# Performance work log

Hardware: AMD Instinct MI355X
Metric: run time of the kernel (lower is better)

Reference implementation:

```python
import jax, jax.numpy as jnp
import numpy as np

N_NODES = 50000
N_EDGES = 800000
N_FEAT = 128
HIDDEN = 128
N_CLASSES = 10
N_GRAPHS = 100


def setup_inputs() -> dict:
    key = jax.random.key(0)
    ks = jax.random.split(key, 16)
    x = jax.random.normal(ks[0], (N_NODES, N_FEAT), dtype=jnp.float32)
    edge_index = jax.random.randint(ks[1], (2, N_EDGES), 0, N_NODES, dtype=jnp.int64)
    batch = jnp.sort(jax.random.randint(ks[2], (N_NODES,), 0, N_GRAPHS, dtype=jnp.int64))

    def glorot(k, fi, fo):
        s = jnp.sqrt(6.0 / (fi + fo)).astype(jnp.float32)
        return jax.random.uniform(k, (fi, fo), jnp.float32, -s, s)

    return {
        "x": x,
        "edge_index": edge_index,
        "batch": batch,
        "W1": glorot(ks[3], N_FEAT, HIDDEN),
        "b1": jnp.zeros((HIDDEN,), jnp.float32),
        "W2": glorot(ks[4], HIDDEN, HIDDEN),
        "b2": jnp.zeros((HIDDEN,), jnp.float32),
        "W3": glorot(ks[5], HIDDEN, HIDDEN // 2),
        "b3": jnp.zeros((HIDDEN // 2,), jnp.float32),
        "Wf1": glorot(ks[6], HIDDEN // 2, 32),
        "bf1": jnp.zeros((32,), jnp.float32),
        "Wf2": glorot(ks[7], 32, N_CLASSES),
        "bf2": jnp.zeros((N_CLASSES,), jnp.float32),
    }


def _gcn_conv(x, row, col, norm, W, b, n_nodes):
    # GCNConv: x' = D^{-1/2}(A+I)D^{-1/2} (x W) + b
    h = x @ W                                            # [N, out]
    msg = h[row] * norm[:, None]                         # gather + scale per edge
    out = jax.ops.segment_sum(msg, col, num_segments=n_nodes)  # scatter-add to targets
    return out + b


def reference(x, edge_index, batch, W1, b1, W2, b2, W3, b3, Wf1, bf1, Wf2, bf2):
    n = x.shape[0]
    # add self-loops (PyG GCNConv default)
    loop = jnp.arange(n, dtype=edge_index.dtype)
    row = jnp.concatenate([edge_index[0], loop])
    col = jnp.concatenate([edge_index[1], loop])
    # symmetric normalization from in-degree at targets (edge_weight = 1)
    deg = jax.ops.segment_sum(jnp.ones_like(col, x.dtype), col, num_segments=n)
    dinv = jnp.where(deg > 0, jax.lax.rsqrt(deg), 0.0)
    norm = dinv[row] * dinv[col]                         # [E + N]

    h = jax.nn.relu(_gcn_conv(x, row, col, norm, W1, b1, n))
    h = jax.nn.relu(_gcn_conv(h, row, col, norm, W2, b2, n))
    h = jax.nn.relu(_gcn_conv(h, row, col, norm, W3, b3, n))

    # global_mean_pool over graphs
    sums = jax.ops.segment_sum(h, batch, num_segments=N_GRAPHS)
    cnts = jax.ops.segment_sum(jnp.ones((n,), h.dtype), batch, num_segments=N_GRAPHS)
    pooled = sums / jnp.maximum(cnts, 1.0)[:, None]      # [G, hidden//2]

    h = jax.nn.relu(pooled @ Wf1 + bf1)
    logits = h @ Wf2 + bf2                               # [G, num_classes]
    return logits
```

## Files before the change

kernel.cpp:

```cpp
#include <hip/hip_runtime.h>
#include <hip/hip_fp16.h>


#define NGRAPH 100
#define CAP 64

typedef _Float16 f16x8 __attribute__((ext_vector_type(8)));
typedef float f32x4 __attribute__((ext_vector_type(4)));


__global__ __launch_bounds__(256) void prep_all(const float* __restrict__ W1,
                                                const float* __restrict__ W2,
                                                const float* __restrict__ W3,
                                                __half* __restrict__ Wt1,
                                                __half* __restrict__ Wt2,
                                                __half* __restrict__ Wt3,
                                                int* __restrict__ cnt,
                                                float* __restrict__ pooled, int n) {
    const int idx = blockIdx.x * 256 + threadIdx.x;
    if (idx < 16384) {
        int nn = idx >> 7, k = idx & 127;
        Wt1[idx] = __float2half(W1[k * 128 + nn]);
    } else if (idx < 32768) {
        int j = idx - 16384;
        int nn = j >> 7, k = j & 127;
        Wt2[j] = __float2half(W2[k * 128 + nn]);
    } else if (idx < 40960) {
        int j = idx - 32768;
        int nn = j >> 7, k = j & 127;
        Wt3[j] = __float2half(W3[k * 64 + nn]);
    }
    if (idx < n) cnt[idx] = 0;
    if (idx < NGRAPH * 64) pooled[idx] = 0.0f;
}


__global__ void fill_bucket(const int* __restrict__ row, const int* __restrict__ col,
                            int* __restrict__ cnt, int* __restrict__ bucket,
                            int E, int colsPerGroup) {
    const int g  = blockIdx.x & 7;
    const int gb = blockIdx.x >> 3;
    const int nb = gridDim.x >> 3;
    const int lo = g * colsPerGroup, hi = lo + colsPerGroup;
    for (int e = gb * 256 + threadIdx.x; e < E; e += nb * 256) {
        int c = col[e];
        if (c >= lo && c < hi) {
            int pos = atomicAdd(&cnt[c], 1);
            bucket[c * CAP + pos] = row[e];
        }
    }
}


template <int OUT, bool F16IN>
__global__ __launch_bounds__(256) void gemm_mfma(const void* __restrict__ Xv,
                                                 const __half* __restrict__ Wt,
                                                 const float* __restrict__ bias_in,
                                                 const int* __restrict__ cnt,
                                                 __half* __restrict__ Yh, int n) {
    __shared__ _Float16 Xs[64 * 128];
    __shared__ _Float16 Ws[OUT * 128];
    __shared__ float bs[128];

    const float*  Xf = (const float*)Xv;
    const __half* Xh = (const __half*)Xv;

    const int t = threadIdx.x;
    if (t < 128) bs[t] = (bias_in != nullptr) ? bias_in[t] : 0.0f;
    __syncthreads();

    const int row0 = blockIdx.x * 64;
    const bool do_relu = (bias_in != nullptr);

    for (int c = t; c < 64 * 16; c += 256) {
        const int r = c >> 4, q = c & 15;
        const int gr = row0 + r;
        float vals[8];
        #pragma unroll
        for (int i = 0; i < 8; ++i) vals[i] = 0.0f;
        if (gr < n) {
            if (F16IN) {
                f16x8 hv = *(const f16x8*)&Xh[(size_t)gr * 128 + q * 8];
                #pragma unroll
                for (int i = 0; i < 8; ++i) vals[i] = (float)hv[i];
            } else {
                float4 va = *(const float4*)&Xf[(size_t)gr * 128 + q * 8];
                float4 vb = *(const float4*)&Xf[(size_t)gr * 128 + q * 8 + 4];
                vals[0] = va.x; vals[1] = va.y; vals[2] = va.z; vals[3] = va.w;
                vals[4] = vb.x; vals[5] = vb.y; vals[6] = vb.z; vals[7] = vb.w;
            }
        }
        if (do_relu) {
            const int k = q * 8;
            #pragma unroll
            for (int i = 0; i < 8; ++i) vals[i] = fmaxf(vals[i] + bs[k + i], 0.f);
        }
        f16x8 hv;
        #pragma unroll
        for (int i = 0; i < 8; ++i) hv[i] = (_Float16)vals[i];
        *(f16x8*)&Xs[(size_t)((r << 4) + (q ^ (r & 15))) * 8] = hv;
    }
    for (int c = t; c < OUT * 16; c += 256) {
        const int nn = c >> 4, q = c & 15;
        f16x8 w = *(const f16x8*)&Wt[nn * 128 + q * 8];
        *(f16x8*)&Ws[(size_t)((nn << 4) + (q ^ (nn & 15))) * 8] = w;
    }
    __syncthreads();

    constexpr int NT = OUT / 16;
    const int lane = t & 63, wave = t >> 6;
    const int m = lane & 15, quad = lane >> 4;

    f32x4 acc[NT];
    #pragma unroll
    for (int i = 0; i < NT; ++i) acc[i] = (f32x4){0.f, 0.f, 0.f, 0.f};

    #pragma unroll
    for (int s = 0; s < 4; ++s) {
        const int qa = s * 4 + quad;
        f16x8 a = *(const f16x8*)&Xs[(size_t)(((wave * 16 + m) << 4) + (qa ^ m)) * 8];
        #pragma unroll
        for (int tt = 0; tt < NT; ++tt) {
            f16x8 b = *(const f16x8*)&Ws[(size_t)(((tt * 16 + m) << 4) + (qa ^ m)) * 8];
            acc[tt] = __builtin_amdgcn_mfma_f32_16x16x32_f16(a, b, acc[tt], 0, 0, 0);
        }
    }

    #pragma unroll
    for (int i = 0; i < 4; ++i) {
        const int gr = row0 + wave * 16 + quad * 4 + i;
        if (gr < n) {
            const float dw = 1.0f / sqrtf((float)(cnt[gr] + 1));
            #pragma unroll
            for (int tt = 0; tt < NT; ++tt)
                Yh[(size_t)gr * OUT + tt * 16 + m] = __float2half(acc[tt][i] * dw);
        }
    }
}


template <int F>
__global__ void gather_kernel(const __half* __restrict__ hs, const int* __restrict__ cnt,
                              const int* __restrict__ bucket,
                              __half* __restrict__ outh, int n) {
    const int lane = threadIdx.x & 63;
    const int c = (blockIdx.x * blockDim.x + threadIdx.x) >> 6;
    if (c >= n) return;
    const int beg = c * CAP;
    const int end = beg + cnt[c];
    const float w = 1.0f / sqrtf((float)(cnt[c] + 1));
    const float2* hq = (const float2*)hs;

    auto cvt = [](float2 raw) {
        __half2 ha = *(__half2*)&raw.x;
        __half2 hb = *(__half2*)&raw.y;
        float2 fa = __half22float2(ha);
        float2 fb = __half22float2(hb);
        return make_float4(fa.x, fa.y, fb.x, fb.y);
    };
    auto pack = [](float4 v) {
        float2 o;
        *(__half2*)&o.x = __float22half2_rn(make_float2(v.x, v.y));
        *(__half2*)&o.y = __float22half2_rn(make_float2(v.z, v.w));
        return o;
    };

    if (F == 128) {
        const int half = lane >> 5;
        const int l    = lane & 31;
        float4 acc = make_float4(0.f, 0.f, 0.f, 0.f);
        if (half == 0) acc = cvt(hq[(size_t)c * 32 + l]);
        int j = beg + half;
        for (; j + 6 < end; j += 8) {
            int s0 = bucket[j], s1 = bucket[j + 2], s2 = bucket[j + 4], s3 = bucket[j + 6];
            float4 v0 = cvt(hq[(size_t)s0 * 32 + l]);
            float4 v1 = cvt(hq[(size_t)s1 * 32 + l]);
            float4 v2 = cvt(hq[(size_t)s2 * 32 + l]);
            float4 v3 = cvt(hq[(size_t)s3 * 32 + l]);
            acc.x += v0.x + v1.x + v2.x + v3.x;
            acc.y += v0.y + v1.y + v2.y + v3.y;
            acc.z += v0.z + v1.z + v2.z + v3.z;
            acc.w += v0.w + v1.w + v2.w + v3.w;
        }
        for (; j < end; j += 2) {
            float4 v = cvt(hq[(size_t)bucket[j] * 32 + l]);
            acc.x += v.x; acc.y += v.y; acc.z += v.z; acc.w += v.w;
        }
        acc.x += __shfl(acc.x, lane ^ 32);
        acc.y += __shfl(acc.y, lane ^ 32);
        acc.z += __shfl(acc.z, lane ^ 32);
        acc.w += __shfl(acc.w, lane ^ 32);
        if (half == 0) {
            float4 o = make_float4(w * acc.x, w * acc.y, w * acc.z, w * acc.w);
            *(float2*)&outh[(size_t)c * 128 + l * 4] = pack(o);
        }
    }
}


__global__ __launch_bounds__(256) void fused_gpool(const __half* __restrict__ hs,
                                                   const int* __restrict__ cnt,
                                                   const int* __restrict__ bucket,
                                                   const float* __restrict__ b3,
                                                   const int* __restrict__ batch,
                                                   float* __restrict__ pooled, int n) {
    const int lane  = threadIdx.x & 63;
    const int half  = lane >> 5;
    const int li    = lane & 31;
    const int wave  = (blockIdx.x * blockDim.x + threadIdx.x) >> 6;
    const int nwav  = (gridDim.x * blockDim.x) >> 6;
    const int chunk = (n + nwav - 1) / nwav;
    const int beg = wave * chunk;
    const int end = min(beg + chunk, n);
    if (beg >= end) return;
    const unsigned* h2 = (const unsigned*)hs;

    auto cvt2 = [](unsigned raw) { return __half22float2(*(__half2*)&raw); };

    const float bias0 = b3[li * 2], bias1 = b3[li * 2 + 1];
    int curg = batch[beg];
    float2 acc = make_float2(0.f, 0.f);
    for (int i = beg; i < end; ++i) {
        int g = batch[i];
        if (g != curg) {
            if (half == 0) {
                atomicAdd(&pooled[curg * 64 + li * 2],     acc.x);
                atomicAdd(&pooled[curg * 64 + li * 2 + 1], acc.y);
            }
            acc = make_float2(0.f, 0.f); curg = g;
        }
        const int deg = cnt[i];
        const float dv = 1.0f / sqrtf((float)(deg + 1));
        float2 sv = make_float2(0.f, 0.f);
        if (half == 0) sv = cvt2(h2[(size_t)i * 32 + li]);
        const int eb = i * CAP, ee = eb + deg;
        int j = eb + half;
        for (; j + 14 < ee; j += 16) {
            int a0 = bucket[j],      a1 = bucket[j + 2],  a2 = bucket[j + 4],  a3 = bucket[j + 6];
            int a4 = bucket[j + 8],  a5 = bucket[j + 10], a6 = bucket[j + 12], a7 = bucket[j + 14];
            float2 v0 = cvt2(h2[(size_t)a0 * 32 + li]);
            float2 v1 = cvt2(h2[(size_t)a1 * 32 + li]);
            float2 v2 = cvt2(h2[(size_t)a2 * 32 + li]);
            float2 v3 = cvt2(h2[(size_t)a3 * 32 + li]);
            float2 v4 = cvt2(h2[(size_t)a4 * 32 + li]);
            float2 v5 = cvt2(h2[(size_t)a5 * 32 + li]);
            float2 v6 = cvt2(h2[(size_t)a6 * 32 + li]);
            float2 v7 = cvt2(h2[(size_t)a7 * 32 + li]);
            sv.x += (v0.x + v1.x) + (v2.x + v3.x) + (v4.x + v5.x) + (v6.x + v7.x);
            sv.y += (v0.y + v1.y) + (v2.y + v3.y) + (v4.y + v5.y) + (v6.y + v7.y);
        }
        for (; j < ee; j += 2) {
            float2 v = cvt2(h2[(size_t)bucket[j] * 32 + li]);
            sv.x += v.x; sv.y += v.y;
        }
        sv.x += __shfl(sv.x, lane ^ 32);
        sv.y += __shfl(sv.y, lane ^ 32);
        acc.x += fmaxf(dv * sv.x + bias0, 0.f);
        acc.y += fmaxf(dv * sv.y + bias1, 0.f);
    }
    if (half == 0) {
        atomicAdd(&pooled[curg * 64 + li * 2],     acc.x);
        atomicAdd(&pooled[curg * 64 + li * 2 + 1], acc.y);
    }
}


__global__ __launch_bounds__(64) void mlp_kernel(const float* __restrict__ pooled,
                                                 const int* __restrict__ batch,
                                                 const float* __restrict__ Wf1,
                                                 const float* __restrict__ bf1,
                                                 const float* __restrict__ Wf2,
                                                 const float* __restrict__ bf2,
                                                 float* __restrict__ out, int n) {
    const int g = blockIdx.x;
    const int t = threadIdx.x;

    auto lb = [&](int v) {
        int lo = 0, hi = n;
        while (lo < hi) { int mid = (lo + hi) >> 1; if (batch[mid] < v) lo = mid + 1; else hi = mid; }
        return lo;
    };
    const int cnt = lb(g + 1) - lb(g);

    __shared__ float pm[64];
    __shared__ float hid[32];

    pm[t] = pooled[g * 64 + t] / (float)(cnt > 0 ? cnt : 1);
    __syncthreads();

    if (t < 32) {
        float a = bf1[t];
        #pragma unroll
        for (int k = 0; k < 64; ++k) a += pm[k] * Wf1[k * 32 + t];
        hid[t] = fmaxf(a, 0.f);
    }
    __syncthreads();

    if (t < 10) {
        float a = bf2[t];
        #pragma unroll
        for (int k = 0; k < 32; ++k) a += hid[k] * Wf2[k * 10 + t];
        out[g * 10 + t] = a;
    }
}


extern "C" void kernel_launch(void* const* d_in, const int* in_sizes, int n_in,
                              void* d_out, int out_size, void* d_ws, size_t ws_size,
                              hipStream_t stream) {
    const float* x     = (const float*)d_in[0];
    const int*   edge  = (const int*)  d_in[1];
    const int*   batch = (const int*)  d_in[2];
    const float* W1    = (const float*)d_in[3];
    const float* b1    = (const float*)d_in[4];
    const float* W2    = (const float*)d_in[5];
    const float* b2    = (const float*)d_in[6];
    const float* W3    = (const float*)d_in[7];
    const float* b3    = (const float*)d_in[8];
    const float* Wf1   = (const float*)d_in[9];
    const float* bf1   = (const float*)d_in[10];
    const float* Wf2   = (const float*)d_in[11];
    const float* bf2   = (const float*)d_in[12];
    float* out = (float*)d_out;

    const int E = in_sizes[1] / 2;
    const int n = in_sizes[2];
    const int* row = edge;
    const int* col = edge + E;

    const int colsPerGroup = (n + 7) / 8;

    const size_t n_pad = ((size_t)n + 64) & ~(size_t)63;
    char* wsb = (char*)d_ws;
    int*    cnt    = (int*)wsb;                  wsb += n_pad * 4;
    float*  pooled = (float*)wsb;                wsb += NGRAPH * 64 * 4;
    int*    bucket = (int*)wsb;                  wsb += (size_t)n_pad * CAP * 4;
    __half* Wt1    = (__half*)wsb;               wsb += 16384 * 2;
    __half* Wt2    = (__half*)wsb;               wsb += 16384 * 2;
    __half* Wt3    = (__half*)wsb;               wsb += 8192 * 2;
    __half* bufA   = (__half*)wsb;               wsb += (size_t)n * 128 * 2;
    __half* bufB   = (__half*)wsb;

    prep_all<<<256, 256, 0, stream>>>(W1, W2, W3, Wt1, Wt2, Wt3, cnt, pooled, n);
    fill_bucket<<<1024, 256, 0, stream>>>(row, col, cnt, bucket, E, colsPerGroup);

    const int ggemm = (n + 63) / 64;
    const int gath_grid = (n * 64 + 255) / 256;

    gemm_mfma<128, false><<<ggemm, 256, 0, stream>>>(x, Wt1, nullptr, cnt, bufA, n);
    gather_kernel<128><<<gath_grid, 256, 0, stream>>>(bufA, cnt, bucket, bufB, n);
    gemm_mfma<128, true><<<ggemm, 256, 0, stream>>>(bufB, Wt2, b1, cnt, bufA, n);
    gather_kernel<128><<<gath_grid, 256, 0, stream>>>(bufA, cnt, bucket, bufB, n);
    gemm_mfma<64, true><<<ggemm, 256, 0, stream>>>(bufB, Wt3, b2, cnt, bufA, n);
    fused_gpool<<<2048, 256, 0, stream>>>(bufA, cnt, bucket, b3, batch, pooled, n);
    mlp_kernel<<<NGRAPH, 64, 0, stream>>>(pooled, batch, Wf1, bf1, Wf2, bf2, out, n);
}
```

Baseline: 278.3 us.

## Split gather into feature-quarter blocks with 4 edge streams per wave

Replaces the per-node gather kernel with a persistent grid-stride kernel. Each 16-lane group handles one quarter of the 128 features (64 bytes per row) for one of four interleaved edge streams, and blockIdx bits pick the quarter so concurrent blocks touch the same feature slice. The aim is more independent loads in flight per wave and better cache locality of the gathered rows. The cost is 4x more waves covering each node, redundant bucket/cnt reads, and narrower 4-byte loads per lane.

```diff
diff --git a/kernel.cpp b/kernel.cpp
--- a/kernel.cpp
+++ b/kernel.cpp
@@ -139,60 +139,52 @@
 }
 
 
-template <int F>
-__global__ void gather_kernel(const __half* __restrict__ hs, const int* __restrict__ cnt,
-                              const int* __restrict__ bucket,
-                              __half* __restrict__ outh, int n) {
+__global__ __launch_bounds__(256) void gather_q128(const __half* __restrict__ hs,
+                                                   const int* __restrict__ cnt,
+                                                   const int* __restrict__ bucket,
+                                                   __half* __restrict__ outh, int n) {
+    const int g    = blockIdx.x & 7;
+    const int q    = g >> 1;
+    const int sub  = g & 1;
+    const int wid  = threadIdx.x >> 6;
     const int lane = threadIdx.x & 63;
-    const int c = (blockIdx.x * blockDim.x + threadIdx.x) >> 6;
-    if (c >= n) return;
-    const int beg = c * CAP;
-    const int end = beg + cnt[c];
-    const float w = 1.0f / sqrtf((float)(cnt[c] + 1));
-    const float2* hq = (const float2*)hs;
-
-    auto cvt = [](float2 raw) {
-        __half2 ha = *(__half2*)&raw.x;
-        __half2 hb = *(__half2*)&raw.y;
-        float2 fa = __half22float2(ha);
-        float2 fb = __half22float2(hb);
-        return make_float4(fa.x, fa.y, fb.x, fb.y);
-    };
-    auto pack = [](float4 v) {
-        float2 o;
-        *(__half2*)&o.x = __float22half2_rn(make_float2(v.x, v.y));
-        *(__half2*)&o.y = __float22half2_rn(make_float2(v.z, v.w));
-        return o;
-    };
-
-    if (F == 128) {
-        const int half = lane >> 5;
-        const int l    = lane & 31;
-        float4 acc = make_float4(0.f, 0.f, 0.f, 0.f);
-        if (half == 0) acc = cvt(hq[(size_t)c * 32 + l]);
-        int j = beg + half;
-        for (; j + 6 < end; j += 8) {
-            int s0 = bucket[j], s1 = bucket[j + 2], s2 = bucket[j + 4], s3 = bucket[j + 6];
-            float4 v0 = cvt(hq[(size_t)s0 * 32 + l]);
-            float4 v1 = cvt(hq[(size_t)s1 * 32 + l]);
-            float4 v2 = cvt(hq[(size_t)s2 * 32 + l]);
-            float4 v3 = cvt(hq[(size_t)s3 * 32 + l]);
-            acc.x += v0.x + v1.x + v2.x + v3.x;
-            acc.y += v0.y + v1.y + v2.y + v3.y;
-            acc.z += v0.z + v1.z + v2.z + v3.z;
-            acc.w += v0.w + v1.w + v2.w + v3.w;
-        }
-        for (; j < end; j += 2) {
-            float4 v = cvt(hq[(size_t)bucket[j] * 32 + l]);
-            acc.x += v.x; acc.y += v.y; acc.z += v.z; acc.w += v.w;
-        }
+    const int strm = lane >> 4;
+    const int li   = lane & 15;
+    const int nwq  = (gridDim.x >> 3) * 4 * 2;
+    const int c0   = ((blockIdx.x >> 3) * 4 + wid) * 2 + sub;
+    const unsigned* h2 = (const unsigned*)hs;
+    unsigned* o2 = (unsigned*)outh;
+    const int qoff = q * 16 + li;
+
+    auto cvt2 = [](unsigned raw) { return __half22float2(*(__half2*)&raw); };
+
+    for (int c = c0; c < n; c += nwq) {
+        const int deg = cnt[c];
+        const float w = 1.0f / sqrtf((float)(deg + 1));
+        float2 acc = make_float2(0.f, 0.f);
+        if (strm == 0) acc = cvt2(h2[(size_t)c * 64 + qoff]);
+        const int jb = c * CAP, je = jb + deg;
+        int j = jb + strm;
+        for (; j + 12 < je; j += 16) {
+            int a0 = bucket[j], a1 = bucket[j + 4], a2 = bucket[j + 8], a3 = bucket[j + 12];
+            float2 v0 = cvt2(h2[(size_t)a0 * 64 + qoff]);
+            float2 v1 = cvt2(h2[(size_t)a1 * 64 + qoff]);
+            float2 v2 = cvt2(h2[(size_t)a2 * 64 + qoff]);
+            float2 v3 = cvt2(h2[(size_t)a3 * 64 + qoff]);
+            acc.x += (v0.x + v1.x) + (v2.x + v3.x);
+            acc.y += (v0.y + v1.y) + (v2.y + v3.y);
+        }
+        for (; j < je; j += 4) {
+            float2 v = cvt2(h2[(size_t)bucket[j] * 64 + qoff]);
+            acc.x += v.x; acc.y += v.y;
+        }
+        acc.x += __shfl(acc.x, lane ^ 16);
+        acc.y += __shfl(acc.y, lane ^ 16);
         acc.x += __shfl(acc.x, lane ^ 32);
         acc.y += __shfl(acc.y, lane ^ 32);
-        acc.z += __shfl(acc.z, lane ^ 32);
-        acc.w += __shfl(acc.w, lane ^ 32);
-        if (half == 0) {
-            float4 o = make_float4(w * acc.x, w * acc.y, w * acc.z, w * acc.w);
-            *(float2*)&outh[(size_t)c * 128 + l * 4] = pack(o);
+        if (strm == 0) {
+            __half2 hv = __float22half2_rn(make_float2(w * acc.x, w * acc.y));
+            o2[(size_t)c * 64 + qoff] = *(unsigned*)&hv;
         }
     }
 }
@@ -345,12 +337,11 @@
     fill_bucket<<<1024, 256, 0, stream>>>(row, col, cnt, bucket, E, colsPerGroup);
 
     const int ggemm = (n + 63) / 64;
-    const int gath_grid = (n * 64 + 255) / 256;
 
     gemm_mfma<128, false><<<ggemm, 256, 0, stream>>>(x, Wt1, nullptr, cnt, bufA, n);
-    gather_kernel<128><<<gath_grid, 256, 0, stream>>>(bufA, cnt, bucket, bufB, n);
+    gather_q128<<<2048, 256, 0, stream>>>(bufA, cnt, bucket, bufB, n);
     gemm_mfma<128, true><<<ggemm, 256, 0, stream>>>(bufB, Wt2, b1, cnt, bufA, n);
-    gather_kernel<128><<<gath_grid, 256, 0, stream>>>(bufA, cnt, bucket, bufB, n);
+    gather_q128<<<2048, 256, 0, stream>>>(bufA, cnt, bucket, bufB, n);
     gemm_mfma<64, true><<<ggemm, 256, 0, stream>>>(bufB, Wt3, b2, cnt, bufA, n);
     fused_gpool<<<2048, 256, 0, stream>>>(bufA, cnt, bucket, b3, batch, pooled, n);
     mlp_kernel<<<NGRAPH, 64, 0, stream>>>(pooled, batch, Wf1, bf1, Wf2, bf2, out, n);
```

Measured after the change: 358.2 us. 1.29x slower.
